# Kernel tuning notes

Hardware: AMD Instinct MI355X
Metric: run time of the kernel (lower is better)

Reference implementation:

```python
import jax, jax.numpy as jnp
import numpy as np

B, T, E, H, V, F = 128, 25, 512, 1024, 10000, 2048


def setup_inputs() -> dict:
    key = jax.random.key(0)
    ks = jax.random.split(key, 32)
    d = {}
    d['tokens'] = jax.random.randint(ks[0], (B, T), 0, V)
    d['features'] = jax.random.normal(ks[1], (B, F), dtype=jnp.float32)
    d['embedding'] = jax.random.normal(ks[2], (V, E), dtype=jnp.float32) * 0.02
    # feature projection (Dropout treated as identity / eval mode)
    d['Wp'] = jax.random.normal(ks[3], (F, H), dtype=jnp.float32) * (1.0 / np.sqrt(F))
    d['bp'] = jnp.zeros((H,), dtype=jnp.float32)
    # layer 0: input_size = E + H  (token embedding ++ projected features)
    in0 = E + H
    std0 = 1.0 / np.sqrt(H + in0)
    i = 4
    for g in ('f', 'i', 'o', 'g'):
        d['W%s0' % g] = jax.random.normal(ks[i], (H + in0, H), dtype=jnp.float32) * std0
        d['b%s0' % g] = jnp.full((H,), 2.0, dtype=jnp.float32)
        i += 1
    # layer 1: input_size = H
    std1 = 1.0 / np.sqrt(H + H)
    for g in ('f', 'i', 'o', 'g'):
        d['W%s1' % g] = jax.random.normal(ks[i], (H + H, H), dtype=jnp.float32) * std1
        d['b%s1' % g] = jnp.full((H,), 2.0, dtype=jnp.float32)
        i += 1
    d['Wout'] = jax.random.normal(ks[i], (H, V), dtype=jnp.float32) * (1.0 / np.sqrt(H))
    d['bout'] = jnp.zeros((V,), dtype=jnp.float32)
    return d


def _lstm_cell(x, h, c, Wf, bf, Wi, bi, Wo, bo, Wg, bg):
    comb = jnp.concatenate([x, h], axis=1)  # [B, in+H]
    f = jax.nn.sigmoid(comb @ Wf + bf)
    i = jax.nn.sigmoid(comb @ Wi + bi)
    o = jax.nn.sigmoid(comb @ Wo + bo)
    g = jnp.tanh(comb @ Wg + bg)
    c_new = f * c + i * g
    h_new = o * jnp.tanh(c_new)
    return h_new, c_new


def reference(tokens, features, embedding, Wp, bp,
              Wf0, bf0, Wi0, bi0, Wo0, bo0, Wg0, bg0,
              Wf1, bf1, Wi1, bi1, Wo1, bo1, Wg1, bg1,
              Wout, bout):
    # feature projection: Dropout(eval) -> Linear -> LeakyReLU
    feat = jax.nn.leaky_relu(features @ Wp + bp)  # [B, H]
    emb = embedding[tokens]                        # [B, T, E]
    emb_t = jnp.transpose(emb, (1, 0, 2))          # [T, B, E] teacher forcing inputs
    z = jnp.zeros((tokens.shape[0], Wf0.shape[1]), dtype=feat.dtype)
    init = (z, z, z, z)  # h0, c0, h1, c1

    def step(carry, x_t):
        h0, c0, h1, c1 = carry
        inp0 = jnp.concatenate([x_t, feat], axis=-1)          # [B, E+H]
        h0n, c0n = _lstm_cell(inp0, h0, c0, Wf0, bf0, Wi0, bi0, Wo0, bo0, Wg0, bg0)
        h1n, c1n = _lstm_cell(h0n, h1, c1, Wf1, bf1, Wi1, bi1, Wo1, bo1, Wg1, bg1)
        return (h0n, c0n, h1n, c1n), h1n

    _, hs = jax.lax.scan(step, init, emb_t)  # [T, B, H]
    logits = jnp.einsum('tbh,hv->tbv', hs, Wout) + bout  # [T, B, V]
    return jnp.transpose(logits, (1, 0, 2))  # [B, T, V] (torch.stack(dim=1))
```

## Files before the change

kernel.cpp:

```cpp
#include <hip/hip_runtime.h>
#include <hip/hip_bf16.h>
#include <cstdint>
#include <cstddef>

constexpr int Bz = 128, Tz = 25, Ez = 512, Hz = 1024, Vz = 10000, Fz = 2048;

typedef unsigned short u16;
typedef __attribute__((ext_vector_type(8))) short bf16x8;
typedef __attribute__((ext_vector_type(4))) float f32x4;

__device__ __forceinline__ float sigm(float x) { return 1.f / (1.f + __expf(-x)); }
__device__ __forceinline__ float tanh_f(float x) {
    float e = __expf(-2.f * x);
    return 2.f / (1.f + e) - 1.f;
}
__device__ __forceinline__ float bf2f(u16 u) {
    return __builtin_bit_cast(float, ((unsigned)u) << 16);
}
__device__ __forceinline__ u16 f2bf(float x) {
    unsigned u = __builtin_bit_cast(unsigned, x);
    u += 0x7fffu + ((u >> 16) & 1u);
    return (u16)(u >> 16);
}
__device__ __forceinline__ void splitbf(float x, u16& h, u16& l) {
    h = f2bf(x);
    l = f2bf(x - bf2f(h));
}

__global__ __launch_bounds__(256) void detect_k(const u16* __restrict__ raw,
                                                int* __restrict__ flag) {
    __shared__ int sbuf[256];
    int tid = threadIdx.x, cnt = 0;
    for (int i = tid; i < 1024; i += 256) {
        u16 u = raw[2 * i];
        int e = (u >> 7) & 0xff;
        if (e >= 110 && e <= 127) cnt++;
    }
    sbuf[tid] = cnt;
    __syncthreads();
    for (int s = 128; s > 0; s >>= 1) {
        if (tid < s) sbuf[tid] += sbuf[tid + s];
        __syncthreads();
    }
    if (tid == 0) flag[0] = (sbuf[0] >= 512) ? 1 : 0;
}

__device__ __forceinline__ float ldf(const void* p, size_t i, int isbf) {
    return isbf ? bf2f(((const u16*)p)[i]) : ((const float*)p)[i];
}

__global__ __launch_bounds__(256) void convf_k(const void* __restrict__ in,
                                               float* __restrict__ out, int n,
                                               const int* __restrict__ flag) {
    int idx = blockIdx.x * 256 + threadIdx.x;
    if (idx >= n) return;
    out[idx] = ldf(in, idx, *flag);
}

__global__ __launch_bounds__(256) void pack2_k(
    const void* __restrict__ bp,
    const void* __restrict__ bf0, const void* __restrict__ bi0,
    const void* __restrict__ bo0, const void* __restrict__ bg0,
    const void* __restrict__ bf1, const void* __restrict__ bi1,
    const void* __restrict__ bo1, const void* __restrict__ bg1,
    const void* __restrict__ bout,
    float* __restrict__ bp_f, float* __restrict__ b0_f, float* __restrict__ b1_f,
    float* __restrict__ bout_f, const int* __restrict__ flag) {
    int idx = blockIdx.x * 256 + threadIdx.x;
    int isbf = *flag;
    if (idx < 1024) {
        bp_f[idx] = ldf(bp, idx, isbf);
    } else if (idx < 5120) {
        int n = idx - 1024, g = n >> 10, j = n & 1023;
        const void* s = (g == 0) ? bf0 : (g == 1) ? bi0 : (g == 2) ? bo0 : bg0;
        b0_f[n] = ldf(s, j, isbf);
    } else if (idx < 9216) {
        int n = idx - 5120, g = n >> 10, j = n & 1023;
        const void* s = (g == 0) ? bf1 : (g == 1) ? bi1 : (g == 2) ? bo1 : bg1;
        b1_f[n] = ldf(s, j, isbf);
    } else if (idx < 9216 + Vz) {
        int n = idx - 9216;
        bout_f[n] = ldf(bout, n, isbf);
    }
}

__global__ __launch_bounds__(256) void gsplit_k(const int* __restrict__ tok,
                                                const void* __restrict__ emb,
                                                u16* __restrict__ Xh,
                                                u16* __restrict__ Xl,
                                                const int* __restrict__ flag) {
    int idx = blockIdx.x * 256 + threadIdx.x;
    if (idx >= 3200 * (Ez / 4)) return;
    int r = idx >> 7, c4 = (idx & 127) << 2;
    int t = r >> 7, b = r & 127;
    int tk = tok[b * Tz + t];
    int isbf = *flag;
    ushort4 h4, l4;
    float v0 = ldf(emb, (size_t)tk * Ez + c4 + 0, isbf);
    float v1 = ldf(emb, (size_t)tk * Ez + c4 + 1, isbf);
    float v2 = ldf(emb, (size_t)tk * Ez + c4 + 2, isbf);
    float v3 = ldf(emb, (size_t)tk * Ez + c4 + 3, isbf);
    splitbf(v0, h4.x, l4.x);
    splitbf(v1, h4.y, l4.y);
    splitbf(v2, h4.z, l4.z);
    splitbf(v3, h4.w, l4.w);
    *(ushort4*)&Xh[(size_t)r * Ez + c4] = h4;
    *(ushort4*)&Xl[(size_t)r * Ez + c4] = l4;
}

__global__ __launch_bounds__(256) void wsplit_k(
    const void* __restrict__ s0, const void* __restrict__ s1,
    const void* __restrict__ s2, const void* __restrict__ s3,
    int K, int Nsrc, u16* __restrict__ Wh, u16* __restrict__ Wl,
    const int* __restrict__ flag) {
    int z = blockIdx.z;
    const void* src = (z == 0) ? s0 : (z == 1) ? s1 : (z == 2) ? s2 : s3;
    __shared__ float tb[32][33];
    int n0 = blockIdx.x * 32, k0 = blockIdx.y * 32, tid = threadIdx.x;
    int isbf = *flag;
    for (int i = 0; i < 4; i++) {
        int idx = i * 256 + tid, rr = idx >> 5, cc = idx & 31;
        int k = k0 + rr, n = n0 + cc;
        tb[rr][cc] = (n < Nsrc) ? ldf(src, (size_t)k * Nsrc + n, isbf) : 0.f;
    }
    __syncthreads();
    size_t dbase = (size_t)z * Nsrc;
    for (int i = 0; i < 4; i++) {
        int idx = i * 256 + tid, rr = idx >> 5, cc = idx & 31;
        int n = n0 + rr, k = k0 + cc;
        u16 hh, ll;
        splitbf(tb[cc][rr], hh, ll);
        size_t o = (dbase + n) * (size_t)K + k;
        Wh[o] = hh;
        Wl[o] = ll;
    }
}

__global__ __launch_bounds__(256) void cellu_k(
    const float* __restrict__ parts, int P,
    const float* __restrict__ add, int astride, int amask,
    float* __restrict__ c,
    u16* __restrict__ hi1, u16* __restrict__ lo1, int ld1,
    u16* __restrict__ hi2, u16* __restrict__ lo2, int ld2) {
    int idx = blockIdx.x * 256 + threadIdx.x;
    int m = idx >> 10, j = idx & 1023;
    size_t ab = (size_t)(m & amask) * astride;
    float gf = add[ab + j];
    float gi = add[ab + 1024 + j];
    float go = add[ab + 2048 + j];
    float gg = add[ab + 3072 + j];
    size_t base = (size_t)m * 4096 + j;
    for (int p = 0; p < P; ++p) {
        const float* pp = parts + (size_t)p * 524288 + base;
        gf += pp[0]; gi += pp[1024]; go += pp[2048]; gg += pp[3072];
    }
    float f = sigm(gf), ii = sigm(gi), o = sigm(go), g = tanh_f(gg);
    float cn = f * c[idx] + ii * g;
    c[idx] = cn;
    float h = o * tanh_f(cn);
    u16 hh, hl;
    splitbf(h, hh, hl);
    size_t o1 = (size_t)m * ld1 + j, o2 = (size_t)m * ld2 + j;
    hi1[o1] = hh; lo1[o1] = hl;
    hi2[o2] = hh; lo2[o2] = hl;
}

template <int ACT, int SPLIT>
__global__ __launch_bounds__(256) void sumPu_k(
    const float* __restrict__ parts, int P, int Ns,
    const float* __restrict__ addv, int astride, int amask,
    float* __restrict__ out, u16* __restrict__ ohi, u16* __restrict__ olo,
    int total) {
    int idx = blockIdx.x * 256 + threadIdx.x;
    if (idx >= total) return;
    int m = idx >> Ns, col = idx & ((1 << Ns) - 1);
    float v = addv[(size_t)(m & amask) * astride + col];
    for (int p = 0; p < P; ++p) v += parts[(size_t)p * total + idx];
    if (ACT == 1) v = (v > 0.f) ? v : 0.01f * v;
    out[idx] = v;
    if (SPLIT) {
        u16 hh, hl;
        splitbf(v, hh, hl);
        ohi[idx] = hh; olo[idx] = hl;
    }
}

__global__ __launch_bounds__(256) void sgemm_part_k(
    const float* __restrict__ A, int lda,
    const void* __restrict__ B0, int ldb,
    float* __restrict__ Cpart, int N, int KC,
    const int* __restrict__ flag) {
    __shared__ float As[16][68];
    __shared__ float Bs[16][68];
    const int tid = threadIdx.x;
    const int tx = tid & 15, ty = tid >> 4;
    const int bn0 = blockIdx.x * 64, bm0 = blockIdx.y * 64;
    const int kbase = blockIdx.z * KC;
    const int isbf = *flag;
    const int ar = tid >> 2, ac4 = (tid & 3) << 2;
    const int bkk = tid >> 4, bn4 = (tid & 15) << 2;

    float acc[4][4];
#pragma unroll
    for (int i = 0; i < 4; i++)
#pragma unroll
        for (int j = 0; j < 4; j++) acc[i][j] = 0.f;

    float4 pa, pb;
    auto loadA = [&](int kt) {
        pa = *(const float4*)(A + (size_t)(bm0 + ar) * lda + kbase + kt + ac4);
    };
    auto loadB = [&](int kt) {
        size_t off = (size_t)(kbase + kt + bkk) * ldb + bn0 + bn4;
        if (isbf) {
            const u16* us = (const u16*)B0 + off;
            pb.x = bf2f(us[0]); pb.y = bf2f(us[1]);
            pb.z = bf2f(us[2]); pb.w = bf2f(us[3]);
        } else {
            pb = *(const float4*)((const float*)B0 + off);
        }
    };

    loadA(0); loadB(0);
    for (int kt = 0; kt < KC; kt += 16) {
        As[ac4 + 0][ar] = pa.x; As[ac4 + 1][ar] = pa.y;
        As[ac4 + 2][ar] = pa.z; As[ac4 + 3][ar] = pa.w;
        *(float4*)&Bs[bkk][bn4] = pb;
        __syncthreads();
        if (kt + 16 < KC) { loadA(kt + 16); loadB(kt + 16); }
#pragma unroll
        for (int kk = 0; kk < 16; ++kk) {
            float a[4], b[4];
            *(float4*)&a[0] = *(const float4*)&As[kk][ty * 4];
            *(float4*)&b[0] = *(const float4*)&Bs[kk][tx * 4];
#pragma unroll
            for (int i = 0; i < 4; ++i)
#pragma unroll
                for (int j = 0; j < 4; ++j)
                    acc[i][j] = fmaf(a[i], b[j], acc[i][j]);
        }
        __syncthreads();
    }
    float* out = Cpart + (size_t)blockIdx.z * 128 * N;
#pragma unroll
    for (int i = 0; i < 4; ++i)
#pragma unroll
        for (int j = 0; j < 4; ++j)
            out[(size_t)(bm0 + ty * 4 + i) * N + bn0 + tx * 4 + j] = acc[i][j];
}

template <int XK>
__global__ __launch_bounds__(256) void rgemm_k(
    const u16* __restrict__ Xh, const u16* __restrict__ Xl, int ldx,
    const u16* __restrict__ Ah, const u16* __restrict__ Al, int ldah,
    const u16* __restrict__ Wh, const u16* __restrict__ Wl, int ldk, int hoff,
    float* __restrict__ parts, int KC) {
    __shared__ u16 sh[15360];
    u16* sAh = sh;
    u16* sAl = sh + 5120;
    u16* sBh = sh + 10240;
    u16* sBl = sh + 12800;
    const int tid = threadIdx.x;
    const int bid = blockIdx.x;
    const int bn0 = (bid & 63) * 64;
    const int z = bid >> 6;
    const int kbase = z * KC;
    const int wid = tid >> 6, lane = tid & 63;
    const int l15 = lane & 15, g = lane >> 4;
    const int wr0 = (wid >> 1) * 64, wc0 = (wid & 1) * 32;

    f32x4 acc[4][2];
#pragma unroll
    for (int mi = 0; mi < 4; ++mi)
#pragma unroll
        for (int nj = 0; nj < 2; ++nj) acc[mi][nj] = (f32x4){0.f, 0.f, 0.f, 0.f};

    int4 pAh[2], pAl[2], pBh, pBl;
    auto stageLoad = [&](int kt) {
#pragma unroll
        for (int it = 0; it < 2; ++it) {
            int idx = it * 256 + tid;
            int row = idx >> 2, kc = (idx & 3) << 3;
            int kg = kbase + kt + kc;
            if (XK > 0 && kg < XK) {
                size_t off = (size_t)row * ldx + kg;
                pAh[it] = *(const int4*)&Xh[off];
                pAl[it] = *(const int4*)&Xl[off];
            } else {
                size_t off = (size_t)row * ldah + (kg - XK);
                pAh[it] = *(const int4*)&Ah[off];
                pAl[it] = *(const int4*)&Al[off];
            }
        }
        {
            int n = tid >> 2, kc = (tid & 3) << 3;
            int kg = kbase + kt + kc;
            int colB = kg + ((XK > 0 && kg < XK) ? 0 : hoff);
            size_t wrow = (size_t)(bn0 + n) * ldk + colB;
            pBh = *(const int4*)&Wh[wrow];
            pBl = *(const int4*)&Wl[wrow];
        }
    };
    auto stageWrite = [&]() {
#pragma unroll
        for (int it = 0; it < 2; ++it) {
            int idx = it * 256 + tid;
            int row = idx >> 2, kc = (idx & 3) << 3;
            *(int4*)&sAh[row * 40 + kc] = pAh[it];
            *(int4*)&sAl[row * 40 + kc] = pAl[it];
        }
        int n = tid >> 2, kc = (tid & 3) << 3;
        *(int4*)&sBh[n * 40 + kc] = pBh;
        *(int4*)&sBl[n * 40 + kc] = pBl;
    };

    stageLoad(0);
    for (int kt = 0; kt < KC; kt += 32) {
        stageWrite();
        __syncthreads();
        if (kt + 32 < KC) stageLoad(kt + 32);
        bf16x8 bh[2], bl[2];
#pragma unroll
        for (int nj = 0; nj < 2; ++nj) {
            int co = (wc0 + nj * 16 + l15) * 40 + 8 * g;
            bh[nj] = *(const bf16x8*)&sBh[co];
            bl[nj] = *(const bf16x8*)&sBl[co];
        }
#pragma unroll
        for (int mi = 0; mi < 4; ++mi) {
            int ar = (wr0 + mi * 16 + l15) * 40 + 8 * g;
            bf16x8 ah = *(const bf16x8*)&sAh[ar];
            bf16x8 al = *(const bf16x8*)&sAl[ar];
#pragma unroll
            for (int nj = 0; nj < 2; ++nj) {
                acc[mi][nj] = __builtin_amdgcn_mfma_f32_16x16x32_bf16(
                    ah, bh[nj], acc[mi][nj], 0, 0, 0);
                acc[mi][nj] = __builtin_amdgcn_mfma_f32_16x16x32_bf16(
                    al, bh[nj], acc[mi][nj], 0, 0, 0);
                acc[mi][nj] = __builtin_amdgcn_mfma_f32_16x16x32_bf16(
                    ah, bl[nj], acc[mi][nj], 0, 0, 0);
            }
        }
        __syncthreads();
    }
    float* outp = parts + (size_t)z * 524288;
#pragma unroll
    for (int mi = 0; mi < 4; ++mi)
#pragma unroll
        for (int nj = 0; nj < 2; ++nj) {
            int col = bn0 + wc0 + nj * 16 + l15;
            int rowb = wr0 + mi * 16 + 4 * g;
#pragma unroll
            for (int r = 0; r < 4; ++r)
                outp[(size_t)(rowb + r) * 4096 + col] = acc[mi][nj][r];
        }
}

__global__ __launch_bounds__(256, 2) void lgemm_k(
    const u16* __restrict__ hs_hi, const u16* __restrict__ hs_lo,
    const u16* __restrict__ Wh, const u16* __restrict__ Wl,
    const float* __restrict__ bout_f, float* __restrict__ out) {
    __shared__ u16 sh[30720];
    u16* sAh = sh;
    u16* sAl = sh + 5120;
    u16* sBh = sh + 10240;
    u16* sBl = sh + 20480;
    const int tid = threadIdx.x;
    const int bn0 = blockIdx.x * 256, bm0 = blockIdx.y * 128;
    const int wid = tid >> 6, lane = tid & 63;
    const int l15 = lane & 15, g = lane >> 4;
    const int wr0 = (wid >> 1) * 64, wc0 = (wid & 1) * 128;

    f32x4 acc[4][8];
#pragma unroll
    for (int mi = 0; mi < 4; ++mi)
#pragma unroll
        for (int nj = 0; nj < 8; ++nj) acc[mi][nj] = (f32x4){0.f, 0.f, 0.f, 0.f};

    int4 pAh[2], pAl[2], pBh[4], pBl[4];
    auto stageLoad = [&](int kt) {
#pragma unroll
        for (int it = 0; it < 2; ++it) {
            int idx = it * 256 + tid;
            int row = idx >> 2, kc = (idx & 3) << 3;
            size_t off = (size_t)(bm0 + row) * Hz + kt + kc;
            pAh[it] = *(const int4*)&hs_hi[off];
            pAl[it] = *(const int4*)&hs_lo[off];
        }
#pragma unroll
        for (int it = 0; it < 4; ++it) {
            int idx = it * 256 + tid;
            int n = idx >> 2, kc = (idx & 3) << 3;
            size_t wr = (size_t)(bn0 + n) * Hz + kt + kc;
            pBh[it] = *(const int4*)&Wh[wr];
            pBl[it] = *(const int4*)&Wl[wr];
        }
    };
    auto stageWrite = [&]() {
#pragma unroll
        for (int it = 0; it < 2; ++it) {
            int idx = it * 256 + tid;
            int row = idx >> 2, kc = (idx & 3) << 3;
            *(int4*)&sAh[row * 40 + kc] = pAh[it];
            *(int4*)&sAl[row * 40 + kc] = pAl[it];
        }
#pragma unroll
        for (int it = 0; it < 4; ++it) {
            int idx = it * 256 + tid;
            int n = idx >> 2, kc = (idx & 3) << 3;
            *(int4*)&sBh[n * 40 + kc] = pBh[it];
            *(int4*)&sBl[n * 40 + kc] = pBl[it];
        }
    };

    stageLoad(0);
    for (int kt = 0; kt < Hz; kt += 32) {
        stageWrite();
        __syncthreads();
        if (kt + 32 < Hz) stageLoad(kt + 32);
#pragma unroll
        for (int half = 0; half < 2; ++half) {
            bf16x8 bh[4], bl[4];
#pragma unroll
            for (int n2 = 0; n2 < 4; ++n2) {
                int co = (wc0 + (half * 4 + n2) * 16 + l15) * 40 + 8 * g;
                bh[n2] = *(const bf16x8*)&sBh[co];
                bl[n2] = *(const bf16x8*)&sBl[co];
            }
#pragma unroll
            for (int mi = 0; mi < 4; ++mi) {
                int ar = (wr0 + mi * 16 + l15) * 40 + 8 * g;
                bf16x8 ah = *(const bf16x8*)&sAh[ar];
                bf16x8 al = *(const bf16x8*)&sAl[ar];
#pragma unroll
                for (int n2 = 0; n2 < 4; ++n2) {
                    int j = half * 4 + n2;
                    acc[mi][j] = __builtin_amdgcn_mfma_f32_16x16x32_bf16(
                        ah, bh[n2], acc[mi][j], 0, 0, 0);
                    acc[mi][j] = __builtin_amdgcn_mfma_f32_16x16x32_bf16(
                        al, bh[n2], acc[mi][j], 0, 0, 0);
                    acc[mi][j] = __builtin_amdgcn_mfma_f32_16x16x32_bf16(
                        ah, bl[n2], acc[mi][j], 0, 0, 0);
                }
            }
        }
        __syncthreads();
    }
#pragma unroll
    for (int mi = 0; mi < 4; ++mi)
#pragma unroll
        for (int nj = 0; nj < 8; ++nj) {
            int col = bn0 + wc0 + nj * 16 + l15;
            if (col < Vz) {
                float bv = bout_f[col];
                int rowb = bm0 + wr0 + mi * 16 + 4 * g;
#pragma unroll
                for (int r = 0; r < 4; ++r) {
                    int grow = rowb + r;
                    int tt = grow >> 7, bb = grow & 127;
                    out[((size_t)(bb * Tz + tt)) * Vz + col] = acc[mi][nj][r] + bv;
                }
            }
        }
}

extern "C" void kernel_launch(void* const* d_in, const int* in_sizes, int n_in,
                              void* d_out, int out_size, void* d_ws, size_t ws_size,
                              hipStream_t stream) {
    const int* tokens = (const int*)d_in[0];
    const void* features = d_in[1];
    const void* embedding = d_in[2];
    const void* Wp = d_in[3];
    const void* bp = d_in[4];
    const void* W0[4] = {d_in[5], d_in[7], d_in[9], d_in[11]};
    const void* b0[4] = {d_in[6], d_in[8], d_in[10], d_in[12]};
    const void* W1[4] = {d_in[13], d_in[15], d_in[17], d_in[19]};
    const void* b1[4] = {d_in[14], d_in[16], d_in[18], d_in[20]};
    const void* Wout = d_in[21];
    const void* bout = d_in[22];

    char* w = (char*)d_ws;
    size_t cur = 0;
    auto alloc = [&](size_t bytes) {
        size_t o = cur;
        cur += (bytes + 255) & ~(size_t)255;
        return o;
    };
    u16* W0h = (u16*)(w + alloc((size_t)4096 * 2560 * 2));
    u16* W0l = (u16*)(w + alloc((size_t)4096 * 2560 * 2));
    u16* W1h = (u16*)(w + alloc((size_t)4096 * 2048 * 2));
    u16* W1l = (u16*)(w + alloc((size_t)4096 * 2048 * 2));
    u16* X0h = (u16*)(w + alloc((size_t)3200 * Ez * 2));
    u16* X0l = (u16*)(w + alloc((size_t)3200 * Ez * 2));
    u16* hs_hi = (u16*)(w + alloc((size_t)3200 * Hz * 2));
    u16* hs_lo = (u16*)(w + alloc((size_t)3200 * Hz * 2));
    float* parts = (float*)(w + alloc((size_t)8 * 524288 * 4));
    float* Sfeat = (float*)(w + alloc((size_t)Bz * 4096 * 4));
    float* featc = (float*)(w + alloc((size_t)Bz * Fz * 4));
    float* featf = (float*)(w + alloc((size_t)Bz * Hz * 4));
    u16* feat_hi = (u16*)(w + alloc((size_t)Bz * Hz * 2));
    u16* feat_lo = (u16*)(w + alloc((size_t)Bz * Hz * 2));
    u16* h0_hi = (u16*)(w + alloc((size_t)Bz * Hz * 2));
    u16* h0_lo = (u16*)(w + alloc((size_t)Bz * Hz * 2));
    u16* comb1_hi = (u16*)(w + alloc((size_t)Bz * 2048 * 2));
    u16* comb1_lo = (u16*)(w + alloc((size_t)Bz * 2048 * 2));
    float* c0 = (float*)(w + alloc((size_t)Bz * Hz * 4));
    float* c1 = (float*)(w + alloc((size_t)Bz * Hz * 4));
    size_t stateBytes = (size_t)Bz * Hz * 2 * 2 + (size_t)Bz * 2048 * 2 * 2 +
                        (size_t)Bz * Hz * 4 * 2;
    float* bp_f = (float*)(w + alloc(1024 * 4));
    float* b0_f = (float*)(w + alloc(4096 * 4));
    float* b1_f = (float*)(w + alloc(4096 * 4));
    float* bout_f = (float*)(w + alloc((size_t)Vz * 4));
    int* dflag = (int*)(w + alloc(256));
    (void)ws_size; (void)in_sizes; (void)n_in; (void)out_size;

    u16* Wouth = W0h;
    u16* Woutl = W0l;

    detect_k<<<1, 256, 0, stream>>>((const u16*)embedding, dflag);

    hipMemsetAsync(h0_hi, 0, stateBytes, stream);

    pack2_k<<<76, 256, 0, stream>>>(bp, b0[0], b0[1], b0[2], b0[3],
                                    b1[0], b1[1], b1[2], b1[3], bout,
                                    bp_f, b0_f, b1_f, bout_f, dflag);
    convf_k<<<1024, 256, 0, stream>>>(features, featc, Bz * Fz, dflag);
    gsplit_k<<<1600, 256, 0, stream>>>(tokens, embedding, X0h, X0l, dflag);
    wsplit_k<<<dim3(32, 80, 4), 256, 0, stream>>>(
        W0[0], W0[1], W0[2], W0[3], 2560, 1024, W0h, W0l, dflag);
    wsplit_k<<<dim3(32, 64, 4), 256, 0, stream>>>(
        W1[0], W1[1], W1[2], W1[3], 2048, 1024, W1h, W1l, dflag);

    sgemm_part_k<<<dim3(16, 2, 4), 256, 0, stream>>>(
        featc, Fz, Wp, Hz, parts, 1024, 512, dflag);
    sumPu_k<1, 1><<<512, 256, 0, stream>>>(parts, 4, 10, bp_f, 0, 0,
                                           featf, feat_hi, feat_lo, Bz * Hz);

    rgemm_k<0><<<512, 256, 0, stream>>>(
        nullptr, nullptr, 0, feat_hi, feat_lo, 1024,
        W0h, W0l, 2560, 512, parts, 128);
    sumPu_k<0, 0><<<2048, 256, 0, stream>>>(parts, 8, 12, b0_f, 0, 0,
                                            Sfeat, nullptr, nullptr, Bz * 4096);

    for (int t = 0; t < Tz; t++) {
        rgemm_k<512><<<512, 256, 0, stream>>>(
            X0h + (size_t)t * 128 * Ez, X0l + (size_t)t * 128 * Ez, Ez,
            h0_hi, h0_lo, 1024, W0h, W0l, 2560, 1024, parts, 192);
        cellu_k<<<512, 256, 0, stream>>>(
            parts, 8, Sfeat, 4096, 127, c0,
            h0_hi, h0_lo, 1024, comb1_hi, comb1_lo, 2048);
        rgemm_k<0><<<512, 256, 0, stream>>>(
            nullptr, nullptr, 0, comb1_hi, comb1_lo, 2048,
            W1h, W1l, 2048, 0, parts, 256);
        cellu_k<<<512, 256, 0, stream>>>(
            parts, 8, b1_f, 0, 0, c1,
            hs_hi + (size_t)t * 128 * Hz, hs_lo + (size_t)t * 128 * Hz, 1024,
            comb1_hi + 1024, comb1_lo + 1024, 2048);
    }

    wsplit_k<<<dim3(320, 32, 1), 256, 0, stream>>>(
        Wout, Wout, Wout, Wout, 1024, Vz, Wouth, Woutl, dflag);

    lgemm_k<<<dim3(40, 25), 256, 0, stream>>>(hs_hi, hs_lo, Wouth, Woutl,
                                              bout_f, (float*)d_out);
}
```

Measured before the change: 2.252 ms.

## Vectorize elementwise kernels, deepen rgemm K-tile, and stage lgemm output through LDS

Several changes land at once. The elementwise cell and sum kernels now process four elements per thread, and the feature projection moves from an FP32 SGEMM to the split-bf16 MFMA rgemm path. rgemm gets a 64-wide K tile with a larger LDS footprint and launch_bounds occupancy 2. lgemm caches A fragments per K step, swizzles its block order, and stages output through LDS for coalesced float4 stores. The larger shared memory in rgemm may reduce occupancy, and Wp and the features are now split to hi/lo bf16 before the projection GEMM.

Result: slower. 3.396 ms (+50.8%).

```diff
diff --git a/kernel.cpp b/kernel.cpp
--- a/kernel.cpp
+++ b/kernel.cpp
@@ -49,12 +49,25 @@
     return isbf ? bf2f(((const u16*)p)[i]) : ((const float*)p)[i];
 }
 
-__global__ __launch_bounds__(256) void convf_k(const void* __restrict__ in,
-                                               float* __restrict__ out, int n,
-                                               const int* __restrict__ flag) {
+__global__ __launch_bounds__(256) void vsplit_k(const void* __restrict__ in,
+                                                u16* __restrict__ oh,
+                                                u16* __restrict__ ol, int n,
+                                                const int* __restrict__ flag) {
     int idx = blockIdx.x * 256 + threadIdx.x;
-    if (idx >= n) return;
-    out[idx] = ldf(in, idx, *flag);
+    int i4 = idx << 2;
+    if (i4 >= n) return;
+    int isbf = *flag;
+    ushort4 h4, l4;
+    float v0 = ldf(in, i4 + 0, isbf);
+    float v1 = ldf(in, i4 + 1, isbf);
+    float v2 = ldf(in, i4 + 2, isbf);
+    float v3 = ldf(in, i4 + 3, isbf);
+    splitbf(v0, h4.x, l4.x);
+    splitbf(v1, h4.y, l4.y);
+    splitbf(v2, h4.z, l4.z);
+    splitbf(v3, h4.w, l4.w);
+    *(ushort4*)&oh[i4] = h4;
+    *(ushort4*)&ol[i4] = l4;
 }
 
 __global__ __launch_bounds__(256) void pack2_k(
@@ -115,155 +128,116 @@
     const int* __restrict__ flag) {
     int z = blockIdx.z;
     const void* src = (z == 0) ? s0 : (z == 1) ? s1 : (z == 2) ? s2 : s3;
-    __shared__ float tb[32][33];
-    int n0 = blockIdx.x * 32, k0 = blockIdx.y * 32, tid = threadIdx.x;
+    __shared__ float tb[64][33];
+    int n0 = blockIdx.x * 32, k0 = blockIdx.y * 64, tid = threadIdx.x;
     int isbf = *flag;
-    for (int i = 0; i < 4; i++) {
-        int idx = i * 256 + tid, rr = idx >> 5, cc = idx & 31;
-        int k = k0 + rr, n = n0 + cc;
-        tb[rr][cc] = (n < Nsrc) ? ldf(src, (size_t)k * Nsrc + n, isbf) : 0.f;
+    for (int i = 0; i < 8; i++) {
+        int idx = i * 256 + tid, k = idx >> 5, n = idx & 31;
+        tb[k][n] = (n0 + n < Nsrc) ? ldf(src, (size_t)(k0 + k) * Nsrc + n0 + n, isbf)
+                                   : 0.f;
     }
     __syncthreads();
     size_t dbase = (size_t)z * Nsrc;
-    for (int i = 0; i < 4; i++) {
-        int idx = i * 256 + tid, rr = idx >> 5, cc = idx & 31;
-        int n = n0 + rr, k = k0 + cc;
+    for (int i = 0; i < 8; i++) {
+        int idx = i * 256 + tid, n = idx >> 6, k = idx & 63;
         u16 hh, ll;
-        splitbf(tb[cc][rr], hh, ll);
-        size_t o = (dbase + n) * (size_t)K + k;
+        splitbf(tb[k][n], hh, ll);
+        size_t o = (dbase + n0 + n) * (size_t)K + k0 + k;
         Wh[o] = hh;
         Wl[o] = ll;
     }
 }
 
 __global__ __launch_bounds__(256) void cellu_k(
-    const float* __restrict__ parts, int P,
+    const float* __restrict__ parts,
     const float* __restrict__ add, int astride, int amask,
     float* __restrict__ c,
     u16* __restrict__ hi1, u16* __restrict__ lo1, int ld1,
     u16* __restrict__ hi2, u16* __restrict__ lo2, int ld2) {
     int idx = blockIdx.x * 256 + threadIdx.x;
-    int m = idx >> 10, j = idx & 1023;
-    size_t ab = (size_t)(m & amask) * astride;
-    float gf = add[ab + j];
-    float gi = add[ab + 1024 + j];
-    float go = add[ab + 2048 + j];
-    float gg = add[ab + 3072 + j];
-    size_t base = (size_t)m * 4096 + j;
-    for (int p = 0; p < P; ++p) {
+    int m = idx >> 8, j4 = (idx & 255) << 2;
+    size_t ab = (size_t)(m & amask) * astride + j4;
+    f32x4 gf = *(const f32x4*)&add[ab];
+    f32x4 gi = *(const f32x4*)&add[ab + 1024];
+    f32x4 go = *(const f32x4*)&add[ab + 2048];
+    f32x4 gg = *(const f32x4*)&add[ab + 3072];
+    size_t base = (size_t)m * 4096 + j4;
+#pragma unroll
+    for (int p = 0; p < 8; ++p) {
         const float* pp = parts + (size_t)p * 524288 + base;
-        gf += pp[0]; gi += pp[1024]; go += pp[2048]; gg += pp[3072];
-    }
-    float f = sigm(gf), ii = sigm(gi), o = sigm(go), g = tanh_f(gg);
-    float cn = f * c[idx] + ii * g;
-    c[idx] = cn;
-    float h = o * tanh_f(cn);
-    u16 hh, hl;
-    splitbf(h, hh, hl);
-    size_t o1 = (size_t)m * ld1 + j, o2 = (size_t)m * ld2 + j;
-    hi1[o1] = hh; lo1[o1] = hl;
-    hi2[o2] = hh; lo2[o2] = hl;
+        gf += *(const f32x4*)&pp[0];
+        gi += *(const f32x4*)&pp[1024];
+        go += *(const f32x4*)&pp[2048];
+        gg += *(const f32x4*)&pp[3072];
+    }
+    int cidx = m * 1024 + j4;
+    f32x4 cv = *(const f32x4*)&c[cidx];
+    ushort4 hh4, hl4;
+    float hv[4];
+#pragma unroll
+    for (int e = 0; e < 4; ++e) {
+        float f = sigm(gf[e]), ii = sigm(gi[e]), o = sigm(go[e]), g = tanh_f(gg[e]);
+        float cn = f * cv[e] + ii * g;
+        cv[e] = cn;
+        hv[e] = o * tanh_f(cn);
+    }
+    *(f32x4*)&c[cidx] = cv;
+    splitbf(hv[0], hh4.x, hl4.x);
+    splitbf(hv[1], hh4.y, hl4.y);
+    splitbf(hv[2], hh4.z, hl4.z);
+    splitbf(hv[3], hh4.w, hl4.w);
+    size_t o1 = (size_t)m * ld1 + j4, o2 = (size_t)m * ld2 + j4;
+    *(ushort4*)&hi1[o1] = hh4;
+    *(ushort4*)&lo1[o1] = hl4;
+    *(ushort4*)&hi2[o2] = hh4;
+    *(ushort4*)&lo2[o2] = hl4;
 }
 
 template <int ACT, int SPLIT>
 __global__ __launch_bounds__(256) void sumPu_k(
-    const float* __restrict__ parts, int P, int Ns,
+    const float* __restrict__ parts, int Ns,
     const float* __restrict__ addv, int astride, int amask,
     float* __restrict__ out, u16* __restrict__ ohi, u16* __restrict__ olo,
     int total) {
     int idx = blockIdx.x * 256 + threadIdx.x;
-    if (idx >= total) return;
-    int m = idx >> Ns, col = idx & ((1 << Ns) - 1);
-    float v = addv[(size_t)(m & amask) * astride + col];
-    for (int p = 0; p < P; ++p) v += parts[(size_t)p * total + idx];
-    if (ACT == 1) v = (v > 0.f) ? v : 0.01f * v;
-    out[idx] = v;
+    int i4 = idx << 2;
+    if (i4 >= total) return;
+    int m = i4 >> Ns, col = i4 & ((1 << Ns) - 1);
+    f32x4 v = *(const f32x4*)&addv[(size_t)(m & amask) * astride + col];
+#pragma unroll
+    for (int p = 0; p < 8; ++p)
+        v += *(const f32x4*)&parts[(size_t)p * total + i4];
+    if (ACT == 1) {
+#pragma unroll
+        for (int e = 0; e < 4; ++e) v[e] = (v[e] > 0.f) ? v[e] : 0.01f * v[e];
+    }
+    *(f32x4*)&out[i4] = v;
     if (SPLIT) {
-        u16 hh, hl;
-        splitbf(v, hh, hl);
-        ohi[idx] = hh; olo[idx] = hl;
-    }
-}
-
-__global__ __launch_bounds__(256) void sgemm_part_k(
-    const float* __restrict__ A, int lda,
-    const void* __restrict__ B0, int ldb,
-    float* __restrict__ Cpart, int N, int KC,
-    const int* __restrict__ flag) {
-    __shared__ float As[16][68];
-    __shared__ float Bs[16][68];
-    const int tid = threadIdx.x;
-    const int tx = tid & 15, ty = tid >> 4;
-    const int bn0 = blockIdx.x * 64, bm0 = blockIdx.y * 64;
-    const int kbase = blockIdx.z * KC;
-    const int isbf = *flag;
-    const int ar = tid >> 2, ac4 = (tid & 3) << 2;
-    const int bkk = tid >> 4, bn4 = (tid & 15) << 2;
-
-    float acc[4][4];
-#pragma unroll
-    for (int i = 0; i < 4; i++)
-#pragma unroll
-        for (int j = 0; j < 4; j++) acc[i][j] = 0.f;
-
-    float4 pa, pb;
-    auto loadA = [&](int kt) {
-        pa = *(const float4*)(A + (size_t)(bm0 + ar) * lda + kbase + kt + ac4);
-    };
-    auto loadB = [&](int kt) {
-        size_t off = (size_t)(kbase + kt + bkk) * ldb + bn0 + bn4;
-        if (isbf) {
-            const u16* us = (const u16*)B0 + off;
-            pb.x = bf2f(us[0]); pb.y = bf2f(us[1]);
-            pb.z = bf2f(us[2]); pb.w = bf2f(us[3]);
-        } else {
-            pb = *(const float4*)((const float*)B0 + off);
-        }
-    };
-
-    loadA(0); loadB(0);
-    for (int kt = 0; kt < KC; kt += 16) {
-        As[ac4 + 0][ar] = pa.x; As[ac4 + 1][ar] = pa.y;
-        As[ac4 + 2][ar] = pa.z; As[ac4 + 3][ar] = pa.w;
-        *(float4*)&Bs[bkk][bn4] = pb;
-        __syncthreads();
-        if (kt + 16 < KC) { loadA(kt + 16); loadB(kt + 16); }
-#pragma unroll
-        for (int kk = 0; kk < 16; ++kk) {
-            float a[4], b[4];
-            *(float4*)&a[0] = *(const float4*)&As[kk][ty * 4];
-            *(float4*)&b[0] = *(const float4*)&Bs[kk][tx * 4];
-#pragma unroll
-            for (int i = 0; i < 4; ++i)
-#pragma unroll
-                for (int j = 0; j < 4; ++j)
-                    acc[i][j] = fmaf(a[i], b[j], acc[i][j]);
-        }
-        __syncthreads();
-    }
-    float* out = Cpart + (size_t)blockIdx.z * 128 * N;
-#pragma unroll
-    for (int i = 0; i < 4; ++i)
-#pragma unroll
-        for (int j = 0; j < 4; ++j)
-            out[(size_t)(bm0 + ty * 4 + i) * N + bn0 + tx * 4 + j] = acc[i][j];
+        ushort4 h4, l4;
+        splitbf(v[0], h4.x, l4.x);
+        splitbf(v[1], h4.y, l4.y);
+        splitbf(v[2], h4.z, l4.z);
+        splitbf(v[3], h4.w, l4.w);
+        *(ushort4*)&ohi[i4] = h4;
+        *(ushort4*)&olo[i4] = l4;
+    }
 }
 
 template <int XK>
-__global__ __launch_bounds__(256) void rgemm_k(
+__global__ __launch_bounds__(256, 2) void rgemm_k(
     const u16* __restrict__ Xh, const u16* __restrict__ Xl, int ldx,
     const u16* __restrict__ Ah, const u16* __restrict__ Al, int ldah,
     const u16* __restrict__ Wh, const u16* __restrict__ Wl, int ldk, int hoff,
-    float* __restrict__ parts, int KC) {
-    __shared__ u16 sh[15360];
+    float* __restrict__ parts, int N, int nbn, int KC) {
+    __shared__ u16 sh[27648];
     u16* sAh = sh;
-    u16* sAl = sh + 5120;
-    u16* sBh = sh + 10240;
-    u16* sBl = sh + 12800;
+    u16* sAl = sh + 9216;
+    u16* sBh = sh + 18432;
+    u16* sBl = sh + 23040;
     const int tid = threadIdx.x;
     const int bid = blockIdx.x;
-    const int bn0 = (bid & 63) * 64;
-    const int z = bid >> 6;
+    const int bn0 = (bid % nbn) * 64;
+    const int z = bid / nbn;
     const int kbase = z * KC;
     const int wid = tid >> 6, lane = tid & 63;
     const int l15 = lane & 15, g = lane >> 4;
@@ -275,12 +249,12 @@
 #pragma unroll
         for (int nj = 0; nj < 2; ++nj) acc[mi][nj] = (f32x4){0.f, 0.f, 0.f, 0.f};
 
-    int4 pAh[2], pAl[2], pBh, pBl;
+    int4 pAh[4], pAl[4], pBh[2], pBl[2];
     auto stageLoad = [&](int kt) {
 #pragma unroll
-        for (int it = 0; it < 2; ++it) {
-            int idx = it * 256 + tid;
-            int row = idx >> 2, kc = (idx & 3) << 3;
+        for (int it = 0; it < 4; ++it) {
+            int idx = it * 256 + tid;
+            int row = idx >> 3, kc = (idx & 7) << 3;
             int kg = kbase + kt + kc;
             if (XK > 0 && kg < XK) {
                 size_t off = (size_t)row * ldx + kg;
@@ -292,58 +266,67 @@
                 pAl[it] = *(const int4*)&Al[off];
             }
         }
-        {
-            int n = tid >> 2, kc = (tid & 3) << 3;
+#pragma unroll
+        for (int it = 0; it < 2; ++it) {
+            int idx = it * 256 + tid;
+            int n = idx >> 3, kc = (idx & 7) << 3;
             int kg = kbase + kt + kc;
             int colB = kg + ((XK > 0 && kg < XK) ? 0 : hoff);
             size_t wrow = (size_t)(bn0 + n) * ldk + colB;
-            pBh = *(const int4*)&Wh[wrow];
-            pBl = *(const int4*)&Wl[wrow];
+            pBh[it] = *(const int4*)&Wh[wrow];
+            pBl[it] = *(const int4*)&Wl[wrow];
         }
     };
     auto stageWrite = [&]() {
 #pragma unroll
+        for (int it = 0; it < 4; ++it) {
+            int idx = it * 256 + tid;
+            int row = idx >> 3, kc = (idx & 7) << 3;
+            *(int4*)&sAh[row * 72 + kc] = pAh[it];
+            *(int4*)&sAl[row * 72 + kc] = pAl[it];
+        }
+#pragma unroll
         for (int it = 0; it < 2; ++it) {
             int idx = it * 256 + tid;
-            int row = idx >> 2, kc = (idx & 3) << 3;
-            *(int4*)&sAh[row * 40 + kc] = pAh[it];
-            *(int4*)&sAl[row * 40 + kc] = pAl[it];
-        }
-        int n = tid >> 2, kc = (tid & 3) << 3;
-        *(int4*)&sBh[n * 40 + kc] = pBh;
-        *(int4*)&sBl[n * 40 + kc] = pBl;
+            int n = idx >> 3, kc = (idx & 7) << 3;
+            *(int4*)&sBh[n * 72 + kc] = pBh[it];
+            *(int4*)&sBl[n * 72 + kc] = pBl[it];
+        }
     };
 
     stageLoad(0);
-    for (int kt = 0; kt < KC; kt += 32) {
+    for (int kt = 0; kt < KC; kt += 64) {
         stageWrite();
         __syncthreads();
-        if (kt + 32 < KC) stageLoad(kt + 32);
-        bf16x8 bh[2], bl[2];
-#pragma unroll
-        for (int nj = 0; nj < 2; ++nj) {
-            int co = (wc0 + nj * 16 + l15) * 40 + 8 * g;
-            bh[nj] = *(const bf16x8*)&sBh[co];
-            bl[nj] = *(const bf16x8*)&sBl[co];
-        }
-#pragma unroll
-        for (int mi = 0; mi < 4; ++mi) {
-            int ar = (wr0 + mi * 16 + l15) * 40 + 8 * g;
-            bf16x8 ah = *(const bf16x8*)&sAh[ar];
-            bf16x8 al = *(const bf16x8*)&sAl[ar];
+        if (kt + 64 < KC) stageLoad(kt + 64);
+#pragma unroll
+        for (int kh = 0; kh < 2; ++kh) {
+            bf16x8 bh[2], bl[2];
 #pragma unroll
             for (int nj = 0; nj < 2; ++nj) {
-                acc[mi][nj] = __builtin_amdgcn_mfma_f32_16x16x32_bf16(
-                    ah, bh[nj], acc[mi][nj], 0, 0, 0);
-                acc[mi][nj] = __builtin_amdgcn_mfma_f32_16x16x32_bf16(
-                    al, bh[nj], acc[mi][nj], 0, 0, 0);
-                acc[mi][nj] = __builtin_amdgcn_mfma_f32_16x16x32_bf16(
-                    ah, bl[nj], acc[mi][nj], 0, 0, 0);
-            }
-        }
-        __syncthreads();
-    }
-    float* outp = parts + (size_t)z * 524288;
+                int co = (wc0 + nj * 16 + l15) * 72 + 32 * kh + 8 * g;
+                bh[nj] = *(const bf16x8*)&sBh[co];
+                bl[nj] = *(const bf16x8*)&sBl[co];
+            }
+#pragma unroll
+            for (int mi = 0; mi < 4; ++mi) {
+                int ar = (wr0 + mi * 16 + l15) * 72 + 32 * kh + 8 * g;
+                bf16x8 ah = *(const bf16x8*)&sAh[ar];
+                bf16x8 al = *(const bf16x8*)&sAl[ar];
+#pragma unroll
+                for (int nj = 0; nj < 2; ++nj) {
+                    acc[mi][nj] = __builtin_amdgcn_mfma_f32_16x16x32_bf16(
+                        ah, bh[nj], acc[mi][nj], 0, 0, 0);
+                    acc[mi][nj] = __builtin_amdgcn_mfma_f32_16x16x32_bf16(
+                        al, bh[nj], acc[mi][nj], 0, 0, 0);
+                    acc[mi][nj] = __builtin_amdgcn_mfma_f32_16x16x32_bf16(
+                        ah, bl[nj], acc[mi][nj], 0, 0, 0);
+                }
+            }
+        }
+        __syncthreads();
+    }
+    float* outp = parts + (size_t)z * 128 * N;
 #pragma unroll
     for (int mi = 0; mi < 4; ++mi)
 #pragma unroll
@@ -352,7 +335,7 @@
             int rowb = wr0 + mi * 16 + 4 * g;
 #pragma unroll
             for (int r = 0; r < 4; ++r)
-                outp[(size_t)(rowb + r) * 4096 + col] = acc[mi][nj][r];
+                outp[(size_t)(rowb + r) * N + col] = acc[mi][nj][r];
         }
 }
 
@@ -365,8 +348,10 @@
     u16* sAl = sh + 5120;
     u16* sBh = sh + 10240;
     u16* sBl = sh + 20480;
+    float* fsh = (float*)sh;
     const int tid = threadIdx.x;
-    const int bn0 = blockIdx.x * 256, bm0 = blockIdx.y * 128;
+    int wg = (blockIdx.x & 7) * 125 + (blockIdx.x >> 3);
+    const int bn0 = (wg / 25) * 256, bm0 = (wg % 25) * 128;
     const int wid = tid >> 6, lane = tid & 63;
     const int l15 = lane & 15, g = lane >> 4;
     const int wr0 = (wid >> 1) * 64, wc0 = (wid & 1) * 128;
@@ -418,6 +403,13 @@
         stageWrite();
         __syncthreads();
         if (kt + 32 < Hz) stageLoad(kt + 32);
+        bf16x8 ahv[4], alv[4];
+#pragma unroll
+        for (int mi = 0; mi < 4; ++mi) {
+            int ar = (wr0 + mi * 16 + l15) * 40 + 8 * g;
+            ahv[mi] = *(const bf16x8*)&sAh[ar];
+            alv[mi] = *(const bf16x8*)&sAl[ar];
+        }
 #pragma unroll
         for (int half = 0; half < 2; ++half) {
             bf16x8 bh[4], bl[4];
@@ -429,39 +421,63 @@
             }
 #pragma unroll
             for (int mi = 0; mi < 4; ++mi) {
-                int ar = (wr0 + mi * 16 + l15) * 40 + 8 * g;
-                bf16x8 ah = *(const bf16x8*)&sAh[ar];
-                bf16x8 al = *(const bf16x8*)&sAl[ar];
 #pragma unroll
                 for (int n2 = 0; n2 < 4; ++n2) {
                     int j = half * 4 + n2;
                     acc[mi][j] = __builtin_amdgcn_mfma_f32_16x16x32_bf16(
-                        ah, bh[n2], acc[mi][j], 0, 0, 0);
+                        ahv[mi], bh[n2], acc[mi][j], 0, 0, 0);
                     acc[mi][j] = __builtin_amdgcn_mfma_f32_16x16x32_bf16(
-                        al, bh[n2], acc[mi][j], 0, 0, 0);
+                        alv[mi], bh[n2], acc[mi][j], 0, 0, 0);
                     acc[mi][j] = __builtin_amdgcn_mfma_f32_16x16x32_bf16(
-                        ah, bl[n2], acc[mi][j], 0, 0, 0);
+                        ahv[mi], bl[n2], acc[mi][j], 0, 0, 0);
                 }
             }
         }
         __syncthreads();
     }
-#pragma unroll
-    for (int mi = 0; mi < 4; ++mi)
-#pragma unroll
-        for (int nj = 0; nj < 8; ++nj) {
-            int col = bn0 + wc0 + nj * 16 + l15;
-            if (col < Vz) {
-                float bv = bout_f[col];
-                int rowb = bm0 + wr0 + mi * 16 + 4 * g;
-#pragma unroll
-                for (int r = 0; r < 4; ++r) {
-                    int grow = rowb + r;
-                    int tt = grow >> 7, bb = grow & 127;
-                    out[((size_t)(bb * Tz + tt)) * Vz + col] = acc[mi][nj][r] + bv;
+
+#define FIDX(lr, col) ((lr)*264 + ((col) >> 5) * 33 + ((col)&31))
+#pragma unroll 1
+    for (int p = 0; p < 4; ++p) {
+        __syncthreads();
+#pragma unroll
+        for (int mi = 0; mi < 4; ++mi) {
+            int gr = wr0 + mi * 16;
+            if (gr >= p * 32 && gr < p * 32 + 32) {
+                int lr0 = gr - p * 32 + 4 * g;
+#pragma unroll
+                for (int nj = 0; nj < 8; ++nj) {
+                    int col = wc0 + nj * 16 + l15;
+#pragma unroll
+                    for (int r = 0; r < 4; ++r)
+                        fsh[FIDX(lr0 + r, col)] = acc[mi][nj][r];
                 }
             }
         }
+        __syncthreads();
+#pragma unroll
+        for (int sub = 0; sub < 2; ++sub) {
+            int lr = sub * 16 + (tid >> 4);
+            int cb = (tid & 15) * 4;
+            int grow = bm0 + p * 32 + lr;
+            int tt = grow >> 7, bb = grow & 127;
+            size_t obase = ((size_t)(bb * Tz + tt)) * Vz;
+#pragma unroll
+            for (int j = 0; j < 4; ++j) {
+                int col = cb + 64 * j;
+                int gcol = bn0 + col;
+                if (gcol < Vz) {
+                    float4 v;
+                    v.x = fsh[FIDX(lr, col + 0)] + bout_f[gcol + 0];
+                    v.y = fsh[FIDX(lr, col + 1)] + bout_f[gcol + 1];
+                    v.z = fsh[FIDX(lr, col + 2)] + bout_f[gcol + 2];
+                    v.w = fsh[FIDX(lr, col + 3)] + bout_f[gcol + 3];
+                    *(float4*)&out[obase + gcol] = v;
+                }
+            }
+        }
+    }
+#undef FIDX
 }
 
 extern "C" void kernel_launch(void* const* d_in, const int* in_sizes, int n_in,
@@ -496,7 +512,6 @@
     u16* hs_lo = (u16*)(w + alloc((size_t)3200 * Hz * 2));
     float* parts = (float*)(w + alloc((size_t)8 * 524288 * 4));
     float* Sfeat = (float*)(w + alloc((size_t)Bz * 4096 * 4));
-    float* featc = (float*)(w + alloc((size_t)Bz * Fz * 4));
     float* featf = (float*)(w + alloc((size_t)Bz * Hz * 4));
     u16* feat_hi = (u16*)(w + alloc((size_t)Bz * Hz * 2));
     u16* feat_lo = (u16*)(w + alloc((size_t)Bz * Hz * 2));
@@ -517,6 +532,10 @@
 
     u16* Wouth = W0h;
     u16* Woutl = W0l;
+    u16* Wpth = hs_hi;
+    u16* Wptl = hs_lo;
+    u16* fc_hi = (u16*)Sfeat;
+    u16* fc_lo = fc_hi + (size_t)Bz * Fz;
 
     detect_k<<<1, 256, 0, stream>>>((const u16*)embedding, dflag);
 
@@ -525,43 +544,46 @@
     pack2_k<<<76, 256, 0, stream>>>(bp, b0[0], b0[1], b0[2], b0[3],
                                     b1[0], b1[1], b1[2], b1[3], bout,
                                     bp_f, b0_f, b1_f, bout_f, dflag);
-    convf_k<<<1024, 256, 0, stream>>>(features, featc, Bz * Fz, dflag);
+    vsplit_k<<<256, 256, 0, stream>>>(features, fc_hi, fc_lo, Bz * Fz, dflag);
     gsplit_k<<<1600, 256, 0, stream>>>(tokens, embedding, X0h, X0l, dflag);
-    wsplit_k<<<dim3(32, 80, 4), 256, 0, stream>>>(
+    wsplit_k<<<dim3(32, 40, 4), 256, 0, stream>>>(
         W0[0], W0[1], W0[2], W0[3], 2560, 1024, W0h, W0l, dflag);
-    wsplit_k<<<dim3(32, 64, 4), 256, 0, stream>>>(
+    wsplit_k<<<dim3(32, 32, 4), 256, 0, stream>>>(
         W1[0], W1[1], W1[2], W1[3], 2048, 1024, W1h, W1l, dflag);
-
-    sgemm_part_k<<<dim3(16, 2, 4), 256, 0, stream>>>(
-        featc, Fz, Wp, Hz, parts, 1024, 512, dflag);
-    sumPu_k<1, 1><<<512, 256, 0, stream>>>(parts, 4, 10, bp_f, 0, 0,
+    wsplit_k<<<dim3(32, 32, 1), 256, 0, stream>>>(
+        Wp, Wp, Wp, Wp, 2048, 1024, Wpth, Wptl, dflag);
+
+    rgemm_k<0><<<128, 256, 0, stream>>>(
+        nullptr, nullptr, 0, fc_hi, fc_lo, 2048,
+        Wpth, Wptl, 2048, 0, parts, 1024, 16, 256);
+    sumPu_k<1, 1><<<128, 256, 0, stream>>>(parts, 10, bp_f, 0, 0,
                                            featf, feat_hi, feat_lo, Bz * Hz);
 
     rgemm_k<0><<<512, 256, 0, stream>>>(
         nullptr, nullptr, 0, feat_hi, feat_lo, 1024,
-        W0h, W0l, 2560, 512, parts, 128);
-    sumPu_k<0, 0><<<2048, 256, 0, stream>>>(parts, 8, 12, b0_f, 0, 0,
-                                            Sfeat, nullptr, nullptr, Bz * 4096);
+        W0h, W0l, 2560, 512, parts, 4096, 64, 128);
+    sumPu_k<0, 0><<<512, 256, 0, stream>>>(parts, 12, b0_f, 0, 0,
+                                           Sfeat, nullptr, nullptr, Bz * 4096);
 
     for (int t = 0; t < Tz; t++) {
         rgemm_k<512><<<512, 256, 0, stream>>>(
             X0h + (size_t)t * 128 * Ez, X0l + (size_t)t * 128 * Ez, Ez,
-            h0_hi, h0_lo, 1024, W0h, W0l, 2560, 1024, parts, 192);
-        cellu_k<<<512, 256, 0, stream>>>(
-            parts, 8, Sfeat, 4096, 127, c0,
+            h0_hi, h0_lo, 1024, W0h, W0l, 2560, 1024, parts, 4096, 64, 192);
+        cellu_k<<<128, 256, 0, stream>>>(
+            parts, Sfeat, 4096, 127, c0,
             h0_hi, h0_lo, 1024, comb1_hi, comb1_lo, 2048);
         rgemm_k<0><<<512, 256, 0, stream>>>(
             nullptr, nullptr, 0, comb1_hi, comb1_lo, 2048,
-            W1h, W1l, 2048, 0, parts, 256);
-        cellu_k<<<512, 256, 0, stream>>>(
-            parts, 8, b1_f, 0, 0, c1,
+            W1h, W1l, 2048, 0, parts, 4096, 64, 256);
+        cellu_k<<<128, 256, 0, stream>>>(
+            parts, b1_f, 0, 0, c1,
             hs_hi + (size_t)t * 128 * Hz, hs_lo + (size_t)t * 128 * Hz, 1024,
             comb1_hi + 1024, comb1_lo + 1024, 2048);
     }
 
-    wsplit_k<<<dim3(320, 32, 1), 256, 0, stream>>>(
+    wsplit_k<<<dim3(320, 16, 1), 256, 0, stream>>>(
         Wout, Wout, Wout, Wout, 1024, Vz, Wouth, Woutl, dflag);
 
-    lgemm_k<<<dim3(40, 25), 256, 0, stream>>>(hs_hi, hs_lo, Wouth, Woutl,
-                                              bout_f, (float*)d_out);
-}
+    lgemm_k<<<1000, 256, 0, stream>>>(hs_hi, hs_lo, Wouth, Woutl,
+                                      bout_f, (float*)d_out);
+}
```
